# Optimization experiments

Hardware: AMD Instinct MI355X
Metric: run time of the kernel (lower is better)

Reference implementation:

```python
import jax, jax.numpy as jnp
import numpy as np

NUM_NODES = 100000
EMB = 128
NUM_RELS = 18
BATCH = 1024


def setup_inputs() -> dict:
    key = jax.random.key(0)
    k1, k2, k3, k4 = jax.random.split(key, 4)
    # parameters initialized like torch.rand -> uniform [0, 1)
    embeddings = jax.random.uniform(k1, (NUM_NODES, EMB), dtype=jnp.float32)
    relations = jax.random.uniform(k2, (NUM_RELS, EMB), dtype=jnp.float32)
    batch_subj_index = jax.random.randint(k3, (BATCH,), 0, NUM_NODES, dtype=jnp.int64)
    rel_index = jax.random.randint(k4, (BATCH,), 0, NUM_RELS, dtype=jnp.int64)
    return {
        "batch_subj_index": batch_subj_index,
        "rel_index": rel_index,
        "embeddings": embeddings,
        "relations": relations,
    }


def reference(batch_subj_index, rel_index, embeddings, relations):
    # DistMult full-table scoring (batch_obj_index is None branch).
    # torch: (subj_emb * rel_emb * emb[:, None, :]).sum(-1).T  -> [B, N]
    # Same math, expressed as precombine + single contraction.
    subj_emb = embeddings[batch_subj_index]          # [B, E]
    rel_emb = relations[rel_index]                   # [B, E]
    combined = subj_emb * rel_emb                    # [B, E]
    scores = jnp.einsum("be,ne->bn", combined, embeddings)  # [B, N]
    return scores
```

## Files before the change

kernel.cpp:

```cpp
#include <hip/hip_runtime.h>
#include <hip/hip_bf16.h>

namespace {
constexpr int NODES = 100000;
constexpr int EMBD  = 128;
constexpr int BATCH = 1024;
constexpr int STRIP = 160;
constexpr int NI    = 10;
constexpr int NPASS = 8;
constexpr int NBLK  = NODES / STRIP;
constexpr int NXCD  = 8;
}

typedef __attribute__((ext_vector_type(8))) short bf16x8_t;
typedef __attribute__((ext_vector_type(4))) float f32x4_t;

__device__ __forceinline__ short f2bf(float f) {
    __hip_bfloat16 h = __float2bfloat16(f);
    short s; __builtin_memcpy(&s, &h, 2); return s;
}

__global__ void combine_kernel(const int* __restrict__ subj,
                               const int* __restrict__ rel,
                               const float* __restrict__ emb,
                               const float* __restrict__ rels,
                               short* __restrict__ out) {
    const int b = blockIdx.x;
    const int t = threadIdx.x;
    const float v = emb[(size_t)subj[b] * EMBD + t] * rels[rel[b] * EMBD + t];
    out[b * EMBD + t] = f2bf(v);
}

__global__ __launch_bounds__(256, 3) void distmult_kernel(
        const short* __restrict__ A,
        const float* __restrict__ B,
        float* __restrict__ C) {
    __shared__ short Bs[STRIP * EMBD];

    const int bid = (int)blockIdx.x;
    const int xcd = bid % NXCD;
    const int idx = bid / NXCD;
    constexpr int q = NBLK / NXCD;
    constexpr int r = NBLK % NXCD;
    const int strip = (xcd < r ? xcd * (q + 1) : r * (q + 1) + (xcd - r) * q) + idx;
    const int n0  = strip * STRIP;
    const int tid = (int)threadIdx.x;

#pragma unroll
    for (int c = 0; c < 10; ++c) {
        const int e = (c * 256 + tid) * 8;
        const int rr = e >> 7;
        const int k  = e & 127;
        const float* p = B + (size_t)(n0 + rr) * EMBD + k;
        f32x4_t lo = *reinterpret_cast<const f32x4_t*>(p);
        f32x4_t hi = *reinterpret_cast<const f32x4_t*>(p + 4);
        bf16x8_t v;
#pragma unroll
        for (int j = 0; j < 4; ++j) { v[j] = f2bf(lo[j]); v[4 + j] = f2bf(hi[j]); }
        const int byteaddr = rr * 256 + ((k * 2) ^ ((rr & 7) << 4));
        *reinterpret_cast<bf16x8_t*>(reinterpret_cast<char*>(Bs) + byteaddr) = v;
    }
    __syncthreads();

    const int w  = tid >> 6;
    const int l  = tid & 63;
    const int fr = l & 15;
    const int fq = l >> 4;
    const int swz = (fr & 7) << 4;
    const char* BsBase = reinterpret_cast<const char*>(Bs) + fr * 256;

#pragma unroll
    for (int p = 0; p < NPASS; ++p) {
        const int m0 = p * 128 + w * 32;
        bf16x8_t a[2][4];
#pragma unroll
        for (int mi = 0; mi < 2; ++mi) {
            const short* qp = A + (m0 + mi * 16 + fr) * EMBD + fq * 8;
#pragma unroll
            for (int kk = 0; kk < 4; ++kk)
                a[mi][kk] = *reinterpret_cast<const bf16x8_t*>(qp + kk * 32);
        }

        f32x4_t acc[2][NI] = {};
#pragma unroll
        for (int kk = 0; kk < 4; ++kk) {
#pragma unroll
            for (int h = 0; h < 2; ++h) {
                bf16x8_t bfr[5];
#pragma unroll
                for (int j = 0; j < 5; ++j) {
                    const int ni = h * 5 + j;
                    const int byteoff = ni * 4096 + ((kk * 64 + fq * 16) ^ swz);
                    bfr[j] = *reinterpret_cast<const bf16x8_t*>(BsBase + byteoff);
                }
#pragma unroll
                for (int mi = 0; mi < 2; ++mi)
#pragma unroll
                    for (int j = 0; j < 5; ++j)
                        acc[mi][h * 5 + j] = __builtin_amdgcn_mfma_f32_16x16x32_bf16(
                            bfr[j], a[mi][kk], acc[mi][h * 5 + j], 0, 0, 0);
            }
        }

#pragma unroll
        for (int mi = 0; mi < 2; ++mi) {
            const size_t rowoff = (size_t)(m0 + mi * 16 + fr) * NODES;
#pragma unroll
            for (int ni = 0; ni < NI; ++ni)
                *reinterpret_cast<f32x4_t*>(C + rowoff + n0 + ni * 16 + fq * 4) =
                    acc[mi][ni];
        }
    }
}

extern "C" void kernel_launch(void* const* d_in, const int* in_sizes, int n_in,
                              void* d_out, int out_size, void* d_ws, size_t ws_size,
                              hipStream_t stream) {
    const int*   subj = (const int*)d_in[0];
    const int*   rel  = (const int*)d_in[1];
    const float* emb  = (const float*)d_in[2];
    const float* rels = (const float*)d_in[3];
    float* out = (float*)d_out;
    short* combined = (short*)d_ws;

    combine_kernel<<<BATCH, EMBD, 0, stream>>>(subj, rel, emb, rels, combined);
    distmult_kernel<<<NBLK, 256, 0, stream>>>(combined, emb, out);
}
```

Measured before the change: 114.9 us.

## Use 512 blocks with variable-width 192/208-node strips to balance CUs

Replaces the fixed 625 blocks of 160-node strips with exactly 512 blocks whose strips are 192 or 208 nodes wide, chosen by a closed-form start formula. Each block dispatches to a templated body specialised for its width. Shared memory becomes dynamic, and launch bounds drop to 2 blocks per CU. The goal is to remove the partial second wave and tail imbalance across the 256 CUs. The cost is larger per-block register and LDS footprint, and the XCD-aware strip remapping is dropped.

Measured after the change: 186.7 us. +62.5%, slower.

```diff
diff --git a/kernel.cpp b/kernel.cpp
--- a/kernel.cpp
+++ b/kernel.cpp
@@ -5,11 +5,9 @@
 constexpr int NODES = 100000;
 constexpr int EMBD  = 128;
 constexpr int BATCH = 1024;
-constexpr int STRIP = 160;
-constexpr int NI    = 10;
 constexpr int NPASS = 8;
-constexpr int NBLK  = NODES / STRIP;
-constexpr int NXCD  = 8;
+constexpr int NBLK  = 512;
+constexpr int NWIDE = 106;
 }
 
 typedef __attribute__((ext_vector_type(8))) short bf16x8_t;
@@ -18,6 +16,10 @@
 __device__ __forceinline__ short f2bf(float f) {
     __hip_bfloat16 h = __float2bfloat16(f);
     short s; __builtin_memcpy(&s, &h, 2); return s;
+}
+
+__device__ __forceinline__ int strip_start(int bid) {
+    return 192 * bid + 16 * ((bid * NWIDE) >> 9);
 }
 
 __global__ void combine_kernel(const int* __restrict__ subj,
@@ -31,23 +33,15 @@
     out[b * EMBD + t] = f2bf(v);
 }
 
-__global__ __launch_bounds__(256, 3) void distmult_kernel(
-        const short* __restrict__ A,
-        const float* __restrict__ B,
-        float* __restrict__ C) {
-    __shared__ short Bs[STRIP * EMBD];
-
-    const int bid = (int)blockIdx.x;
-    const int xcd = bid % NXCD;
-    const int idx = bid / NXCD;
-    constexpr int q = NBLK / NXCD;
-    constexpr int r = NBLK % NXCD;
-    const int strip = (xcd < r ? xcd * (q + 1) : r * (q + 1) + (xcd - r) * q) + idx;
-    const int n0  = strip * STRIP;
-    const int tid = (int)threadIdx.x;
+template <int W>
+__device__ __forceinline__ void block_body(const short* __restrict__ A,
+                                           const float* __restrict__ B,
+                                           float* __restrict__ C,
+                                           short* Bs, int n0, int tid) {
+    constexpr int NI = W / 16;
 
 #pragma unroll
-    for (int c = 0; c < 10; ++c) {
+    for (int c = 0; c < NI; ++c) {
         const int e = (c * 256 + tid) * 8;
         const int rr = e >> 7;
         const int k  = e & 127;
@@ -85,20 +79,24 @@
 #pragma unroll
         for (int kk = 0; kk < 4; ++kk) {
 #pragma unroll
-            for (int h = 0; h < 2; ++h) {
+            for (int base = 0; base < NI; base += 5) {
+                constexpr int REM = 0;  (void)REM;
                 bf16x8_t bfr[5];
 #pragma unroll
                 for (int j = 0; j < 5; ++j) {
-                    const int ni = h * 5 + j;
-                    const int byteoff = ni * 4096 + ((kk * 64 + fq * 16) ^ swz);
-                    bfr[j] = *reinterpret_cast<const bf16x8_t*>(BsBase + byteoff);
+                    if (base + j < NI) {
+                        const int ni = base + j;
+                        const int byteoff = ni * 4096 + ((kk * 64 + fq * 16) ^ swz);
+                        bfr[j] = *reinterpret_cast<const bf16x8_t*>(BsBase + byteoff);
+                    }
                 }
 #pragma unroll
                 for (int mi = 0; mi < 2; ++mi)
 #pragma unroll
                     for (int j = 0; j < 5; ++j)
-                        acc[mi][h * 5 + j] = __builtin_amdgcn_mfma_f32_16x16x32_bf16(
-                            bfr[j], a[mi][kk], acc[mi][h * 5 + j], 0, 0, 0);
+                        if (base + j < NI)
+                            acc[mi][base + j] = __builtin_amdgcn_mfma_f32_16x16x32_bf16(
+                                bfr[j], a[mi][kk], acc[mi][base + j], 0, 0, 0);
             }
         }
 
@@ -113,6 +111,19 @@
     }
 }
 
+__global__ __launch_bounds__(256, 2) void distmult_kernel(
+        const short* __restrict__ A,
+        const float* __restrict__ B,
+        float* __restrict__ C) {
+    extern __shared__ short Bs[];
+    const int bid = (int)blockIdx.x;
+    const int n0 = strip_start(bid);
+    const int wdt = strip_start(bid + 1) - n0;
+    const int tid = (int)threadIdx.x;
+    if (wdt == 208) block_body<208>(A, B, C, Bs, n0, tid);
+    else            block_body<192>(A, B, C, Bs, n0, tid);
+}
+
 extern "C" void kernel_launch(void* const* d_in, const int* in_sizes, int n_in,
                               void* d_out, int out_size, void* d_ws, size_t ws_size,
                               hipStream_t stream) {
@@ -124,5 +135,6 @@
     short* combined = (short*)d_ws;
 
     combine_kernel<<<BATCH, EMBD, 0, stream>>>(subj, rel, emb, rels, combined);
-    distmult_kernel<<<NBLK, 256, 0, stream>>>(combined, emb, out);
+    distmult_kernel<<<NBLK, 256, 208 * EMBD * sizeof(short), stream>>>(
+        combined, emb, out);
 }
```
